# Kernel optimization log

Hardware: AMD Instinct MI355X
Metric: run time of the kernel (lower is better)

## Reference

```python
import jax, jax.numpy as jnp
import numpy as np

B, C, D, H, W = 4, 256, 16, 16, 16
REDUCTION = 8
CR = C // REDUCTION  # q/k channel dim = 32


def setup_inputs() -> dict:
    key = jax.random.key(0)
    k1, k2, k3, k4, k5, k6 = jax.random.split(key, 6)
    x = jax.random.normal(k1, (B, C, D, H, W), dtype=jnp.float32)
    # 1x1x1 conv weights are just [out_ch, in_ch] matrices
    Wq = jax.random.normal(k2, (CR, C), dtype=jnp.float32) * (1.0 / np.sqrt(C))
    Wk = jax.random.normal(k3, (CR, C), dtype=jnp.float32) * (1.0 / np.sqrt(C))
    Wv = jax.random.normal(k4, (C, C), dtype=jnp.float32) * (1.0 / np.sqrt(C))
    Wo = jax.random.normal(k5, (C, C), dtype=jnp.float32) * (1.0 / np.sqrt(C))
    gamma = jnp.zeros((1,), dtype=jnp.float32) + 0.5  # nonzero so output depends on attention
    return {"x": x, "Wq": Wq, "Wk": Wk, "Wv": Wv, "Wo": Wo, "gamma": gamma}


def reference(x, Wq, Wk, Wv, Wo, gamma):
    b, c, d, h, w = x.shape
    n = d * h * w
    scale = Wq.shape[0] ** -0.5  # (channels // reduction) ** -0.5
    xf = x.reshape(b, c, n)                      # [B, C, N]
    q = jnp.einsum('oc,bcn->bon', Wq, xf)        # [B, CR, N]
    k = jnp.einsum('oc,bcn->bon', Wk, xf)        # [B, CR, N]
    v = jnp.einsum('oc,bcn->bon', Wv, xf)        # [B, C, N]
    attn = jax.nn.softmax(jnp.einsum('bcn,bcm->bnm', q, k) * scale, axis=-1)  # [B, N, N]
    out = jnp.einsum('bcm,bnm->bcn', v, attn)    # v @ attn^T -> [B, C, N]
    out = jnp.einsum('oc,bcn->bon', Wo, out)     # output 1x1x1 conv
    out = out.reshape(b, c, d, h, w)
    return gamma[0] * out + x
```

## Files before the change

kernel.cpp:

```cpp
#include <hip/hip_runtime.h>
#include <hip/hip_bf16.h>

#define BATCH 4
#define CH 256
#define CRD 32
#define NN 4096

typedef __bf16 bf16x8 __attribute__((ext_vector_type(8)));
typedef float floatx4 __attribute__((ext_vector_type(4)));
typedef float floatx16 __attribute__((ext_vector_type(16)));
typedef unsigned short ushort4v __attribute__((ext_vector_type(4)));
typedef unsigned short ushort8v __attribute__((ext_vector_type(8)));
typedef unsigned int uint2v __attribute__((ext_vector_type(2)));
typedef unsigned int uint4v __attribute__((ext_vector_type(4)));

static __device__ __forceinline__ unsigned short f2bf(float f) {
    __bf16 h = (__bf16)f;
    return __builtin_bit_cast(unsigned short, h);
}
static __device__ __forceinline__ float bf2f(unsigned short h) {
    return __uint_as_float((unsigned int)h << 16);
}


__global__ __launch_bounds__(256) void wconv_kernel(
    const float* __restrict__ Wq, const float* __restrict__ Wk,
    const float* __restrict__ Wv, const float* __restrict__ Wo,
    unsigned short* __restrict__ What, unsigned short* __restrict__ WobF)
{
    const int o = blockIdx.x;
    const int t = threadIdx.x;
    float scale = 1.0f;
    const float* src;
    if (o < 32)      { src = Wq + o * 256;
                       scale = 0.17677669529663687f * 1.4426950408889634f; }
    else if (o < 64) { src = Wk + (o - 32) * 256; }
    else             { src = Wv + (o - 64) * 256; }
    const int mb = o >> 5;
    const size_t idx = ((size_t)(mb * 16 + (t >> 4)) * 64
                        + (o & 31) + 32 * ((t >> 3) & 1)) * 8 + (t & 7);
    What[idx] = f2bf(src[t] * scale);
    if (o < 256) {
        const size_t i2 = ((size_t)((o >> 5) * 16 + (t >> 4)) * 64
                           + (o & 31) + 32 * ((t >> 3) & 1)) * 8 + (t & 7);
        WobF[i2] = f2bf(Wo[o * 256 + t]);
    }
}

static __device__ __forceinline__ uint4v hmerge(
    const ushort4v& xp, const ushort4v& yp, int h)
{
    uint2v xd = __builtin_bit_cast(uint2v, xp);
    uint2v yd = __builtin_bit_cast(uint2v, yp);
    unsigned int px0 = (unsigned int)__shfl_xor((int)xd[0], 32);
    unsigned int px1 = (unsigned int)__shfl_xor((int)xd[1], 32);
    unsigned int py0 = (unsigned int)__shfl_xor((int)yd[0], 32);
    unsigned int py1 = (unsigned int)__shfl_xor((int)yd[1], 32);
    uint4v st;
    st[0] = h ? py0 : xd[0];
    st[1] = h ? py1 : xd[1];
    st[2] = h ? yd[0] : px0;
    st[3] = h ? yd[1] : px1;
    return st;
}

__global__ __launch_bounds__(640, 4) void qkv_kernel(
    const float* __restrict__ x, const unsigned short* __restrict__ What,
    unsigned short* __restrict__ qh, unsigned short* __restrict__ kh,
    unsigned short* __restrict__ vh)
{
    __shared__ __align__(16) unsigned short xf[16 * 512];

    const int t = threadIdx.x;
    const int w = t >> 6;
    const int l = t & 63;
    const int l31 = l & 31;
    const int h = l >> 5;
    const int nt = blockIdx.x, b = blockIdx.y;
    const int n0 = nt * 32;

    if (t < 512) {
        const float* xb = x + (size_t)(b * CH) * NN + n0;
        const int n = t & 31;
        const int cq = t >> 5;
        #pragma unroll
        for (int p = 0; p < 4; ++p) {
            int c = p * 64 + cq * 4;
            float v0 = xb[(size_t)(c + 0) * NN + n];
            float v1 = xb[(size_t)(c + 1) * NN + n];
            float v2 = xb[(size_t)(c + 2) * NN + n];
            float v3 = xb[(size_t)(c + 3) * NN + n];
            ushort4v u4;
            u4[0] = f2bf(v0); u4[1] = f2bf(v1); u4[2] = f2bf(v2); u4[3] = f2bf(v3);
            int addr = ((4 * p + (cq >> 2)) * 64 + n + 32 * ((cq >> 1) & 1)) * 8
                       + 4 * (cq & 1);
            *(ushort4v*)&xf[addr] = u4;
        }
    }
    __syncthreads();

    floatx16 acc;
    #pragma unroll
    for (int i = 0; i < 16; ++i) acc[i] = 0.f;

    for (int kblk = 0; kblk < 16; ++kblk) {
        bf16x8 bf = *(const bf16x8*)&xf[kblk * 512 + l * 8];
        bf16x8 af = *(const bf16x8*)(What + ((size_t)(w * 16 + kblk) * 64 + l) * 8);
        acc = __builtin_amdgcn_mfma_f32_32x32x16_bf16(af, bf, acc, 0, 0, 0);
    }

    auto store_qk = [&](unsigned short* dst, const floatx16& a) {
        size_t base = (size_t)(b * 128 + nt) * 1024;
        #pragma unroll
        for (int sb = 0; sb < 2; ++sb) {
            ushort4v xp, yp;
            #pragma unroll
            for (int i = 0; i < 4; ++i) {
                xp[i] = f2bf(a[8 * sb + i]);
                yp[i] = f2bf(a[8 * sb + 4 + i]);
            }
            uint4v st = hmerge(xp, yp, h);
            *(uint4v*)(dst + base + (size_t)sb * 512 + (size_t)l * 8) = st;
        }
    };

    if (w == 0)      store_qk(qh, acc);
    else if (w == 1) store_qk(kh, acc);

    __syncthreads();

    if (w >= 2) {
        const int cblk = w - 2;
        const int chunk = cblk * 2 + (l31 >> 4);
        const int hib = (l31 >> 3) & 1;
        #pragma unroll
        for (int r = 0; r < 16; ++r) {
            int rowo = (r & 3) + 8 * (r >> 2) + 4 * h;
            int unit = chunk * 64 + hib * 32 + rowo;
            int pu = unit ^ ((unit >> 5) & 7);
            xf[pu * 8 + (l31 & 7)] = f2bf(acc[r]);
        }
    }

    __syncthreads();

    if (t < 512) {
        #pragma unroll
        for (int p = 0; p < 2; ++p) {
            int Lu = p * 512 + t;
            int pu = Lu ^ ((Lu >> 5) & 7);
            uint4v d = *(const uint4v*)&xf[pu * 8];
            int chunk = Lu >> 6;
            int cblk = chunk >> 1, sub = chunk & 1;
            size_t dst = (((size_t)b * 8 + cblk) * 256 + nt * 2 + sub) * 512
                         + (size_t)(Lu & 63) * 8;
            *(uint4v*)(vh + dst) = d;
        }
    }
}

#define SM_M0 12.0f

__global__ __launch_bounds__(512, 4) void attn_kernel(
    const unsigned short* __restrict__ qh, const unsigned short* __restrict__ kh,
    const unsigned short* __restrict__ vh, unsigned short* __restrict__ Opart,
    float* __restrict__ ml)
{
    __shared__ unsigned short p_lds[2 * 16 * 64 * 8];
    __shared__ float psum_s[8][32];

    const int t = threadIdx.x;
    const int w = t >> 6;
    const int l = t & 63;
    const int l31 = l & 31;
    const int h = l >> 5;
    const int wk = w & 3;
    const int hq = w >> 2;

    const int lin = blockIdx.x + ((int)blockIdx.y << 6) + ((int)blockIdx.z << 7);
    const int combo = lin & 7;
    const int gp = lin >> 3;
    const int ks = combo & 1;
    const int b  = combo >> 1;
    const int g0 = 2 * gp, g1 = 2 * gp + 1;

    const unsigned short* qB = qh + (size_t)(b * 128 + (hq ? g1 : g0)) * 1024;
    const unsigned short* kB = kh + (size_t)b * 128 * 1024;
    const unsigned short* vB = vh + (size_t)b * 8 * 256 * 512;

    bf16x8 qf0 = *(const bf16x8*)(qB + l * 8);
    bf16x8 qf1 = *(const bf16x8*)(qB + 512 + l * 8);

    bf16x8 kf0 = *(const bf16x8*)(kB + (size_t)(ks * 64 + wk) * 1024 + l * 8);
    bf16x8 kf1 = *(const bf16x8*)(kB + (size_t)(ks * 64 + wk) * 1024 + 512 + l * 8);

    float l_loc = 0.f;
    floatx16 acc_a, acc_b;
    #pragma unroll
    for (int i = 0; i < 16; ++i) { acc_a[i] = 0.f; acc_b[i] = 0.f; }

    for (int it = 0; it < 16; ++it) {
        const int pbase = (it & 1) << 13;

        floatx16 sacc;
        #pragma unroll
        for (int i = 0; i < 16; ++i) sacc[i] = 0.f;
        __builtin_amdgcn_s_setprio(1);
        sacc = __builtin_amdgcn_mfma_f32_32x32x16_bf16(kf0, qf0, sacc, 0, 0, 0);
        sacc = __builtin_amdgcn_mfma_f32_32x32x16_bf16(kf1, qf1, sacc, 0, 0, 0);
        __builtin_amdgcn_s_setprio(0);

        float pv[16];
        #pragma unroll
        for (int r = 0; r < 16; ++r) pv[r] = __builtin_exp2f(sacc[r] - SM_M0);
        float s0 = (pv[0] + pv[1]) + (pv[2] + pv[3]);
        float s1 = (pv[4] + pv[5]) + (pv[6] + pv[7]);
        float s2 = (pv[8] + pv[9]) + (pv[10] + pv[11]);
        float s3 = (pv[12] + pv[13]) + (pv[14] + pv[15]);
        l_loc += (s0 + s1) + (s2 + s3);
        #pragma unroll
        for (int rg = 0; rg < 4; ++rg) {
            ushort4v pk;
            #pragma unroll
            for (int i = 0; i < 4; ++i) pk[i] = f2bf(pv[rg * 4 + i]);
            int idx = pbase
                    + ((hq * 8 + 2 * wk + (rg >> 1)) * 64
                       + l31 + 32 * (rg & 1)) * 8 + 4 * h;
            *(ushort4v*)&p_lds[idx] = pk;
        }
        if (it < 15) {
            const unsigned short* kn = kB + (size_t)(ks * 64 + (it + 1) * 4 + wk) * 1024;
            kf0 = *(const bf16x8*)(kn + l * 8);
            kf1 = *(const bf16x8*)(kn + 512 + l * 8);
        }
        const unsigned short* v0b = vB + ((size_t)w * 256 + (ks * 16 + it) * 8) * 512;
        bf16x8 va0 = *(const bf16x8*)(v0b + 0 * 512 + l * 8);
        bf16x8 va1 = *(const bf16x8*)(v0b + 1 * 512 + l * 8);
        bf16x8 va2 = *(const bf16x8*)(v0b + 2 * 512 + l * 8);
        bf16x8 va3 = *(const bf16x8*)(v0b + 3 * 512 + l * 8);
        bf16x8 va4 = *(const bf16x8*)(v0b + 4 * 512 + l * 8);
        bf16x8 va5 = *(const bf16x8*)(v0b + 5 * 512 + l * 8);
        bf16x8 va6 = *(const bf16x8*)(v0b + 6 * 512 + l * 8);
        bf16x8 va7 = *(const bf16x8*)(v0b + 7 * 512 + l * 8);

        __syncthreads();

        bf16x8 pa = *(const bf16x8*)&p_lds[pbase + l * 8];
        bf16x8 pb = *(const bf16x8*)&p_lds[pbase + 4096 + l * 8];
        #pragma unroll
        for (int s = 0; s < 8; ++s) {
            bf16x8 vcur = (s == 0) ? va0 : (s == 1) ? va1 : (s == 2) ? va2
                        : (s == 3) ? va3 : (s == 4) ? va4 : (s == 5) ? va5
                        : (s == 6) ? va6 : va7;
            bf16x8 pa_n, pb_n;
            if (s < 7) {
                pa_n = *(const bf16x8*)&p_lds[pbase + ((s + 1) * 64 + l) * 8];
                pb_n = *(const bf16x8*)&p_lds[pbase + 4096 + ((s + 1) * 64 + l) * 8];
            }
            __builtin_amdgcn_s_setprio(1);
            acc_a = __builtin_amdgcn_mfma_f32_32x32x16_bf16(vcur, pa, acc_a, 0, 0, 0);
            acc_b = __builtin_amdgcn_mfma_f32_32x32x16_bf16(vcur, pb, acc_b, 0, 0, 0);
            __builtin_amdgcn_s_setprio(0);
            pa = pa_n; pb = pb_n;
        }
    }

    float lt = l_loc + __shfl_xor(l_loc, 32);
    if (h == 0) psum_s[w][l31] = lt;
    __syncthreads();

    if (w == 0 && h == 0) {
        float l_run = (psum_s[0][l31] + psum_s[1][l31])
                    + (psum_s[2][l31] + psum_s[3][l31]);
        ml[((size_t)(b * 128 + g0) * 2 + ks) * 32 + l31] = l_run;
    }
    if (w == 4 && h == 0) {
        float l_run = (psum_s[4][l31] + psum_s[5][l31])
                    + (psum_s[6][l31] + psum_s[7][l31]);
        ml[((size_t)(b * 128 + g1) * 2 + ks) * 32 + l31] = l_run;
    }

    unsigned short* opa = Opart + ((size_t)((b * 128 + g0) * 2 + ks)) * 8192;
    unsigned short* opb = Opart + ((size_t)((b * 128 + g1) * 2 + ks)) * 8192;
    #pragma unroll
    for (int ct = 0; ct < 2; ++ct) {
        const floatx16& a = ct ? acc_b : acc_a;
        unsigned short* op = ct ? opb : opa;
        #pragma unroll
        for (int sb = 0; sb < 2; ++sb) {
            ushort4v xp, yp;
            #pragma unroll
            for (int i = 0; i < 4; ++i) {
                xp[i] = f2bf(a[8 * sb + i]);
                yp[i] = f2bf(a[8 * sb + 4 + i]);
            }
            uint4v st = hmerge(xp, yp, h);
            int sP = 2 * w + sb;
            *(uint4v*)(op + ((size_t)sP * 64 + l) * 8) = st;
        }
    }
}

__global__ __launch_bounds__(256, 4) void out_kernel(
    const unsigned short* __restrict__ Opart, const float* __restrict__ ml,
    const unsigned short* __restrict__ WobF, const float* __restrict__ x,
    const float* __restrict__ gamma, float* __restrict__ out)
{
    const int t = threadIdx.x;
    const int w = t >> 6;
    const int l = t & 63;
    const int l31 = l & 31;
    const int h = l >> 5;
    const int qt = blockIdx.x, mhalf = blockIdx.y, b = blockIdx.z;
    const int mt = mhalf * 4 + w;

    const size_t slot2 = (size_t)(b * 128 + qt) * 2;
    float l0 = ml[(slot2 + 0) * 32 + l31];
    float l1 = ml[(slot2 + 1) * 32 + l31];
    float rL = 1.0f / (l0 + l1);

    const unsigned short* o0 = Opart + (slot2 + 0) * 8192;
    const unsigned short* o1 = Opart + (slot2 + 1) * 8192;

    floatx16 a0, a1;
    #pragma unroll
    for (int i = 0; i < 16; ++i) { a0[i] = 0.f; a1[i] = 0.f; }

    for (int s = 0; s < 16; ++s) {
        bf16x8 f0 = *(const bf16x8*)(o0 + (s * 64 + l) * 8);
        bf16x8 f1 = *(const bf16x8*)(o1 + (s * 64 + l) * 8);
        bf16x8 af = *(const bf16x8*)(WobF + ((size_t)(mt * 16 + s) * 64 + l) * 8);
        a0 = __builtin_amdgcn_mfma_f32_32x32x16_bf16(af, f0, a0, 0, 0, 0);
        a1 = __builtin_amdgcn_mfma_f32_32x32x16_bf16(af, f1, a1, 0, 0, 0);
    }

    const float gm = gamma[0];
    #pragma unroll
    for (int r = 0; r < 16; ++r) {
        float v = (a0[r] + a1[r]) * rL;
        int o = mt * 32 + (r & 3) + 8 * (r >> 2) + 4 * h;
        int n = qt * 32 + l31;
        size_t oi = ((size_t)(b * 256 + o)) * NN + n;
        out[oi] = gm * v + x[oi];
    }
}

extern "C" void kernel_launch(void* const* d_in, const int* in_sizes, int n_in,
                              void* d_out, int out_size, void* d_ws, size_t ws_size,
                              hipStream_t stream)
{
    const float* x     = (const float*)d_in[0];
    const float* Wq    = (const float*)d_in[1];
    const float* Wk    = (const float*)d_in[2];
    const float* Wv    = (const float*)d_in[3];
    const float* Wo    = (const float*)d_in[4];
    const float* gamma = (const float*)d_in[5];
    float* out = (float*)d_out;

    char* wsb = (char*)d_ws;
    unsigned short* qh    = (unsigned short*)(wsb);
    unsigned short* kh    = (unsigned short*)(wsb + (1u << 20));
    unsigned short* vh    = (unsigned short*)(wsb + (2u << 20));
    unsigned short* What  = (unsigned short*)(wsb + (10u << 20));
    unsigned short* WobF  = (unsigned short*)(wsb + (10u << 20) + (256u << 10));
    unsigned short* Opart = (unsigned short*)(wsb + (11u << 20));
    float*          ml    = (float*)         (wsb + (45u << 20));

    wconv_kernel<<<320, 256, 0, stream>>>(Wq, Wk, Wv, Wo, What, WobF);

    dim3 g1(128, BATCH);
    qkv_kernel<<<g1, 640, 0, stream>>>(x, What, qh, kh, vh);

    dim3 g2(64, 2, BATCH);
    attn_kernel<<<g2, 512, 0, stream>>>(qh, kh, vh, Opart, ml);

    dim3 g3(128, 2, BATCH);
    out_kernel<<<g3, 256, 0, stream>>>(Opart, ml, WobF, x, gamma, out);
}
```

Baseline: 136.9 us.

## Fuse output projection into attention kernel and drop the key-split partials

Removes the two-way key split, so each attention block now loops over all 4096 keys. It normalizes the attention output in registers, stages it in LDS, and applies the Wo projection plus gamma residual directly, eliminating the separate out_kernel and the Opart/ml round trip through global memory. The cost is half as many attention blocks (256 instead of 512) with twice the serial work each. This may reduce parallelism and latency hiding on a large GPU, and the launch-bounds occupancy hint also changes.

```diff
diff --git a/kernel.cpp b/kernel.cpp
--- a/kernel.cpp
+++ b/kernel.cpp
@@ -161,10 +161,11 @@
 
 #define SM_M0 12.0f
 
-__global__ __launch_bounds__(512, 4) void attn_kernel(
+__global__ __launch_bounds__(512, 2) void attn_kernel(
     const unsigned short* __restrict__ qh, const unsigned short* __restrict__ kh,
-    const unsigned short* __restrict__ vh, unsigned short* __restrict__ Opart,
-    float* __restrict__ ml)
+    const unsigned short* __restrict__ vh, const unsigned short* __restrict__ WobF,
+    const float* __restrict__ x, const float* __restrict__ gamma,
+    float* __restrict__ out)
 {
     __shared__ unsigned short p_lds[2 * 16 * 64 * 8];
     __shared__ float psum_s[8][32];
@@ -177,11 +178,9 @@
     const int wk = w & 3;
     const int hq = w >> 2;
 
-    const int lin = blockIdx.x + ((int)blockIdx.y << 6) + ((int)blockIdx.z << 7);
-    const int combo = lin & 7;
-    const int gp = lin >> 3;
-    const int ks = combo & 1;
-    const int b  = combo >> 1;
+    const int lin = blockIdx.x + ((int)blockIdx.y << 6);
+    const int b  = (lin >> 1) & 3;
+    const int gp = ((lin >> 3) << 1) | (lin & 1);
     const int g0 = 2 * gp, g1 = 2 * gp + 1;
 
     const unsigned short* qB = qh + (size_t)(b * 128 + (hq ? g1 : g0)) * 1024;
@@ -191,15 +190,15 @@
     bf16x8 qf0 = *(const bf16x8*)(qB + l * 8);
     bf16x8 qf1 = *(const bf16x8*)(qB + 512 + l * 8);
 
-    bf16x8 kf0 = *(const bf16x8*)(kB + (size_t)(ks * 64 + wk) * 1024 + l * 8);
-    bf16x8 kf1 = *(const bf16x8*)(kB + (size_t)(ks * 64 + wk) * 1024 + 512 + l * 8);
+    bf16x8 kf0 = *(const bf16x8*)(kB + (size_t)wk * 1024 + l * 8);
+    bf16x8 kf1 = *(const bf16x8*)(kB + (size_t)wk * 1024 + 512 + l * 8);
 
     float l_loc = 0.f;
     floatx16 acc_a, acc_b;
     #pragma unroll
     for (int i = 0; i < 16; ++i) { acc_a[i] = 0.f; acc_b[i] = 0.f; }
 
-    for (int it = 0; it < 16; ++it) {
+    for (int it = 0; it < 32; ++it) {
         const int pbase = (it & 1) << 13;
 
         floatx16 sacc;
@@ -228,12 +227,12 @@
                        + l31 + 32 * (rg & 1)) * 8 + 4 * h;
             *(ushort4v*)&p_lds[idx] = pk;
         }
-        if (it < 15) {
-            const unsigned short* kn = kB + (size_t)(ks * 64 + (it + 1) * 4 + wk) * 1024;
+        if (it < 31) {
+            const unsigned short* kn = kB + (size_t)((it + 1) * 4 + wk) * 1024;
             kf0 = *(const bf16x8*)(kn + l * 8);
             kf1 = *(const bf16x8*)(kn + 512 + l * 8);
         }
-        const unsigned short* v0b = vB + ((size_t)w * 256 + (ks * 16 + it) * 8) * 512;
+        const unsigned short* v0b = vB + ((size_t)w * 256 + it * 8) * 512;
         bf16x8 va0 = *(const bf16x8*)(v0b + 0 * 512 + l * 8);
         bf16x8 va1 = *(const bf16x8*)(v0b + 1 * 512 + l * 8);
         bf16x8 va2 = *(const bf16x8*)(v0b + 2 * 512 + l * 8);
@@ -269,79 +268,54 @@
     if (h == 0) psum_s[w][l31] = lt;
     __syncthreads();
 
-    if (w == 0 && h == 0) {
-        float l_run = (psum_s[0][l31] + psum_s[1][l31])
-                    + (psum_s[2][l31] + psum_s[3][l31]);
-        ml[((size_t)(b * 128 + g0) * 2 + ks) * 32 + l31] = l_run;
-    }
-    if (w == 4 && h == 0) {
-        float l_run = (psum_s[4][l31] + psum_s[5][l31])
-                    + (psum_s[6][l31] + psum_s[7][l31]);
-        ml[((size_t)(b * 128 + g1) * 2 + ks) * 32 + l31] = l_run;
-    }
-
-    unsigned short* opa = Opart + ((size_t)((b * 128 + g0) * 2 + ks)) * 8192;
-    unsigned short* opb = Opart + ((size_t)((b * 128 + g1) * 2 + ks)) * 8192;
+    float rLa = 1.0f / ((psum_s[0][l31] + psum_s[1][l31])
+                      + (psum_s[2][l31] + psum_s[3][l31]));
+    float rLb = 1.0f / ((psum_s[4][l31] + psum_s[5][l31])
+                      + (psum_s[6][l31] + psum_s[7][l31]));
+
     #pragma unroll
     for (int ct = 0; ct < 2; ++ct) {
         const floatx16& a = ct ? acc_b : acc_a;
-        unsigned short* op = ct ? opb : opa;
+        const float rL = ct ? rLb : rLa;
+        const int obase = ct ? 8192 : 0;
         #pragma unroll
         for (int sb = 0; sb < 2; ++sb) {
             ushort4v xp, yp;
             #pragma unroll
             for (int i = 0; i < 4; ++i) {
-                xp[i] = f2bf(a[8 * sb + i]);
-                yp[i] = f2bf(a[8 * sb + 4 + i]);
+                xp[i] = f2bf(a[8 * sb + i] * rL);
+                yp[i] = f2bf(a[8 * sb + 4 + i] * rL);
             }
             uint4v st = hmerge(xp, yp, h);
-            int sP = 2 * w + sb;
-            *(uint4v*)(op + ((size_t)sP * 64 + l) * 8) = st;
-        }
-    }
-}
-
-__global__ __launch_bounds__(256, 4) void out_kernel(
-    const unsigned short* __restrict__ Opart, const float* __restrict__ ml,
-    const unsigned short* __restrict__ WobF, const float* __restrict__ x,
-    const float* __restrict__ gamma, float* __restrict__ out)
-{
-    const int t = threadIdx.x;
-    const int w = t >> 6;
-    const int l = t & 63;
-    const int l31 = l & 31;
-    const int h = l >> 5;
-    const int qt = blockIdx.x, mhalf = blockIdx.y, b = blockIdx.z;
-    const int mt = mhalf * 4 + w;
-
-    const size_t slot2 = (size_t)(b * 128 + qt) * 2;
-    float l0 = ml[(slot2 + 0) * 32 + l31];
-    float l1 = ml[(slot2 + 1) * 32 + l31];
-    float rL = 1.0f / (l0 + l1);
-
-    const unsigned short* o0 = Opart + (slot2 + 0) * 8192;
-    const unsigned short* o1 = Opart + (slot2 + 1) * 8192;
-
-    floatx16 a0, a1;
-    #pragma unroll
-    for (int i = 0; i < 16; ++i) { a0[i] = 0.f; a1[i] = 0.f; }
-
-    for (int s = 0; s < 16; ++s) {
-        bf16x8 f0 = *(const bf16x8*)(o0 + (s * 64 + l) * 8);
-        bf16x8 f1 = *(const bf16x8*)(o1 + (s * 64 + l) * 8);
-        bf16x8 af = *(const bf16x8*)(WobF + ((size_t)(mt * 16 + s) * 64 + l) * 8);
-        a0 = __builtin_amdgcn_mfma_f32_32x32x16_bf16(af, f0, a0, 0, 0, 0);
-        a1 = __builtin_amdgcn_mfma_f32_32x32x16_bf16(af, f1, a1, 0, 0, 0);
+            int kblk = 2 * w + sb;
+            *(uint4v*)&p_lds[obase + ((size_t)kblk * 64 + l) * 8] = st;
+        }
+    }
+    __syncthreads();
+
+    floatx16 oa, ob;
+    #pragma unroll
+    for (int i = 0; i < 16; ++i) { oa[i] = 0.f; ob[i] = 0.f; }
+    for (int kblk = 0; kblk < 16; ++kblk) {
+        bf16x8 af = *(const bf16x8*)(WobF + ((size_t)(w * 16 + kblk) * 64 + l) * 8);
+        bf16x8 ba = *(const bf16x8*)&p_lds[((size_t)kblk * 64 + l) * 8];
+        bf16x8 bb = *(const bf16x8*)&p_lds[8192 + ((size_t)kblk * 64 + l) * 8];
+        oa = __builtin_amdgcn_mfma_f32_32x32x16_bf16(af, ba, oa, 0, 0, 0);
+        ob = __builtin_amdgcn_mfma_f32_32x32x16_bf16(af, bb, ob, 0, 0, 0);
     }
 
     const float gm = gamma[0];
     #pragma unroll
-    for (int r = 0; r < 16; ++r) {
-        float v = (a0[r] + a1[r]) * rL;
-        int o = mt * 32 + (r & 3) + 8 * (r >> 2) + 4 * h;
-        int n = qt * 32 + l31;
-        size_t oi = ((size_t)(b * 256 + o)) * NN + n;
-        out[oi] = gm * v + x[oi];
+    for (int ct = 0; ct < 2; ++ct) {
+        const floatx16& a = ct ? ob : oa;
+        const int g = ct ? g1 : g0;
+        #pragma unroll
+        for (int r = 0; r < 16; ++r) {
+            int o = w * 32 + (r & 3) + 8 * (r >> 2) + 4 * h;
+            int n = g * 32 + l31;
+            size_t oi = ((size_t)(b * 256 + o)) * NN + n;
+            out[oi] = gm * a[r] + x[oi];
+        }
     }
 }
 
@@ -363,17 +337,12 @@
     unsigned short* vh    = (unsigned short*)(wsb + (2u << 20));
     unsigned short* What  = (unsigned short*)(wsb + (10u << 20));
     unsigned short* WobF  = (unsigned short*)(wsb + (10u << 20) + (256u << 10));
-    unsigned short* Opart = (unsigned short*)(wsb + (11u << 20));
-    float*          ml    = (float*)         (wsb + (45u << 20));
 
     wconv_kernel<<<320, 256, 0, stream>>>(Wq, Wk, Wv, Wo, What, WobF);
 
     dim3 g1(128, BATCH);
     qkv_kernel<<<g1, 640, 0, stream>>>(x, What, qh, kh, vh);
 
-    dim3 g2(64, 2, BATCH);
-    attn_kernel<<<g2, 512, 0, stream>>>(qh, kh, vh, Opart, ml);
-
-    dim3 g3(128, 2, BATCH);
-    out_kernel<<<g3, 256, 0, stream>>>(Opart, ml, WobF, x, gamma, out);
-}
+    dim3 g2(64, BATCH);
+    attn_kernel<<<g2, 512, 0, stream>>>(qh, kh, vh, WobF, x, gamma, out);
+}
```

Result: no change. 138.9 us (+1.4%).

## Software-pipeline QK^T/softmax one tile ahead of PV accumulation

Applied to the files above, without the earlier changes.

Restructures the attention loop so the QK^T MFMAs, exp2 softmax and P stores to LDS for tile it+1 are issued in the same iteration as the PV MFMAs for tile it. A prologue computes tile 0 before the loop, and the barrier moves to the end of each iteration, so the double-buffered P tile is still protected. The aim is to hide exp/convert latency and the barrier wait behind matrix work and give the scheduler more independent instructions. The cost is higher register pressure from keeping sacc and the V fragments live at the same time, plus one extra barrier.

```diff
diff --git a/kernel.cpp b/kernel.cpp
--- a/kernel.cpp
+++ b/kernel.cpp
@@ -191,25 +191,13 @@
     bf16x8 qf0 = *(const bf16x8*)(qB + l * 8);
     bf16x8 qf1 = *(const bf16x8*)(qB + 512 + l * 8);
 
-    bf16x8 kf0 = *(const bf16x8*)(kB + (size_t)(ks * 64 + wk) * 1024 + l * 8);
-    bf16x8 kf1 = *(const bf16x8*)(kB + (size_t)(ks * 64 + wk) * 1024 + 512 + l * 8);
-
     float l_loc = 0.f;
     floatx16 acc_a, acc_b;
     #pragma unroll
     for (int i = 0; i < 16; ++i) { acc_a[i] = 0.f; acc_b[i] = 0.f; }
 
-    for (int it = 0; it < 16; ++it) {
-        const int pbase = (it & 1) << 13;
-
-        floatx16 sacc;
-        #pragma unroll
-        for (int i = 0; i < 16; ++i) sacc[i] = 0.f;
-        __builtin_amdgcn_s_setprio(1);
-        sacc = __builtin_amdgcn_mfma_f32_32x32x16_bf16(kf0, qf0, sacc, 0, 0, 0);
-        sacc = __builtin_amdgcn_mfma_f32_32x32x16_bf16(kf1, qf1, sacc, 0, 0, 0);
-        __builtin_amdgcn_s_setprio(0);
-
+    auto softmax_store = [&](const floatx16& sacc, int j) {
+        const int pb = (j & 1) << 13;
         float pv[16];
         #pragma unroll
         for (int r = 0; r < 16; ++r) pv[r] = __builtin_exp2f(sacc[r] - SM_M0);
@@ -223,16 +211,43 @@
             ushort4v pk;
             #pragma unroll
             for (int i = 0; i < 4; ++i) pk[i] = f2bf(pv[rg * 4 + i]);
-            int idx = pbase
+            int idx = pb
                     + ((hq * 8 + 2 * wk + (rg >> 1)) * 64
                        + l31 + 32 * (rg & 1)) * 8 + 4 * h;
             *(ushort4v*)&p_lds[idx] = pk;
         }
+    };
+
+    bf16x8 kf0 = *(const bf16x8*)(kB + (size_t)(ks * 64 + wk) * 1024 + l * 8);
+    bf16x8 kf1 = *(const bf16x8*)(kB + (size_t)(ks * 64 + wk) * 1024 + 512 + l * 8);
+    {
+        floatx16 sacc;
+        #pragma unroll
+        for (int i = 0; i < 16; ++i) sacc[i] = 0.f;
+        sacc = __builtin_amdgcn_mfma_f32_32x32x16_bf16(kf0, qf0, sacc, 0, 0, 0);
+        sacc = __builtin_amdgcn_mfma_f32_32x32x16_bf16(kf1, qf1, sacc, 0, 0, 0);
+        softmax_store(sacc, 0);
+    }
+    {
+        const unsigned short* kn = kB + (size_t)(ks * 64 + 4 + wk) * 1024;
+        kf0 = *(const bf16x8*)(kn + l * 8);
+        kf1 = *(const bf16x8*)(kn + 512 + l * 8);
+    }
+    __syncthreads();
+
+    for (int it = 0; it < 16; ++it) {
+        const int pcur = (it & 1) << 13;
+
+        floatx16 sacc;
         if (it < 15) {
-            const unsigned short* kn = kB + (size_t)(ks * 64 + (it + 1) * 4 + wk) * 1024;
-            kf0 = *(const bf16x8*)(kn + l * 8);
-            kf1 = *(const bf16x8*)(kn + 512 + l * 8);
-        }
+            #pragma unroll
+            for (int i = 0; i < 16; ++i) sacc[i] = 0.f;
+            __builtin_amdgcn_s_setprio(1);
+            sacc = __builtin_amdgcn_mfma_f32_32x32x16_bf16(kf0, qf0, sacc, 0, 0, 0);
+            sacc = __builtin_amdgcn_mfma_f32_32x32x16_bf16(kf1, qf1, sacc, 0, 0, 0);
+            __builtin_amdgcn_s_setprio(0);
+        }
+
         const unsigned short* v0b = vB + ((size_t)w * 256 + (ks * 16 + it) * 8) * 512;
         bf16x8 va0 = *(const bf16x8*)(v0b + 0 * 512 + l * 8);
         bf16x8 va1 = *(const bf16x8*)(v0b + 1 * 512 + l * 8);
@@ -243,10 +258,17 @@
         bf16x8 va6 = *(const bf16x8*)(v0b + 6 * 512 + l * 8);
         bf16x8 va7 = *(const bf16x8*)(v0b + 7 * 512 + l * 8);
 
-        __syncthreads();
-
-        bf16x8 pa = *(const bf16x8*)&p_lds[pbase + l * 8];
-        bf16x8 pb = *(const bf16x8*)&p_lds[pbase + 4096 + l * 8];
+        if (it < 15) {
+            softmax_store(sacc, it + 1);
+            if (it < 14) {
+                const unsigned short* kn = kB + (size_t)(ks * 64 + (it + 2) * 4 + wk) * 1024;
+                kf0 = *(const bf16x8*)(kn + l * 8);
+                kf1 = *(const bf16x8*)(kn + 512 + l * 8);
+            }
+        }
+
+        bf16x8 pa = *(const bf16x8*)&p_lds[pcur + l * 8];
+        bf16x8 pb = *(const bf16x8*)&p_lds[pcur + 4096 + l * 8];
         #pragma unroll
         for (int s = 0; s < 8; ++s) {
             bf16x8 vcur = (s == 0) ? va0 : (s == 1) ? va1 : (s == 2) ? va2
@@ -254,8 +276,8 @@
                         : (s == 6) ? va6 : va7;
             bf16x8 pa_n, pb_n;
             if (s < 7) {
-                pa_n = *(const bf16x8*)&p_lds[pbase + ((s + 1) * 64 + l) * 8];
-                pb_n = *(const bf16x8*)&p_lds[pbase + 4096 + ((s + 1) * 64 + l) * 8];
+                pa_n = *(const bf16x8*)&p_lds[pcur + ((s + 1) * 64 + l) * 8];
+                pb_n = *(const bf16x8*)&p_lds[pcur + 4096 + ((s + 1) * 64 + l) * 8];
             }
             __builtin_amdgcn_s_setprio(1);
             acc_a = __builtin_amdgcn_mfma_f32_32x32x16_bf16(vcur, pa, acc_a, 0, 0, 0);
@@ -263,6 +285,8 @@
             __builtin_amdgcn_s_setprio(0);
             pa = pa_n; pb = pb_n;
         }
+
+        __syncthreads();
     }
 
     float lt = l_loc + __shfl_xor(l_loc, 32);
```

After: 136.2 us. No clear change (-0.5%).

## Retile attention to four query tiles per block with four-way key split

Applied to the files above, without the earlier changes.

Each attention block now covers four 32-query tiles and a quarter of the keys, instead of two query tiles and half the keys. Each loaded V fragment therefore feeds four MFMA accumulators rather than two, which halves the total V bytes read from global memory. The cost is twice as many partial outputs and row sums, which the output kernel now reads and reduces across four splits. The software prefetch of the next K tile is also dropped, so K loads now sit on the critical path of each iteration.

```diff
diff --git a/kernel.cpp b/kernel.cpp
--- a/kernel.cpp
+++ b/kernel.cpp
@@ -174,34 +174,35 @@
     const int l = t & 63;
     const int l31 = l & 31;
     const int h = l >> 5;
-    const int wk = w & 3;
-    const int hq = w >> 2;
-
-    const int lin = blockIdx.x + ((int)blockIdx.y << 6) + ((int)blockIdx.z << 7);
-    const int combo = lin & 7;
-    const int gp = lin >> 3;
-    const int ks = combo & 1;
-    const int b  = combo >> 1;
-    const int g0 = 2 * gp, g1 = 2 * gp + 1;
-
-    const unsigned short* qB = qh + (size_t)(b * 128 + (hq ? g1 : g0)) * 1024;
+    const int qq = w >> 1;
+    const int kslc = w & 1;
+
+    const int lin = blockIdx.x + ((int)blockIdx.y << 5) + ((int)blockIdx.z << 7);
+    const int slot = lin >> 3;
+    const int combo = ((lin & 7) << 1) | (slot >> 5);
+    const int qt = slot & 31;
+    const int ks = combo & 3;
+    const int b  = combo >> 2;
+
+    const unsigned short* qB = qh + (size_t)(b * 128 + qt * 4 + qq) * 1024;
     const unsigned short* kB = kh + (size_t)b * 128 * 1024;
     const unsigned short* vB = vh + (size_t)b * 8 * 256 * 512;
 
     bf16x8 qf0 = *(const bf16x8*)(qB + l * 8);
     bf16x8 qf1 = *(const bf16x8*)(qB + 512 + l * 8);
 
-    bf16x8 kf0 = *(const bf16x8*)(kB + (size_t)(ks * 64 + wk) * 1024 + l * 8);
-    bf16x8 kf1 = *(const bf16x8*)(kB + (size_t)(ks * 64 + wk) * 1024 + 512 + l * 8);
-
     float l_loc = 0.f;
-    floatx16 acc_a, acc_b;
-    #pragma unroll
-    for (int i = 0; i < 16; ++i) { acc_a[i] = 0.f; acc_b[i] = 0.f; }
+    floatx16 acc0, acc1, acc2, acc3;
+    #pragma unroll
+    for (int i = 0; i < 16; ++i) { acc0[i] = 0.f; acc1[i] = 0.f;
+                                   acc2[i] = 0.f; acc3[i] = 0.f; }
 
     for (int it = 0; it < 16; ++it) {
         const int pbase = (it & 1) << 13;
 
+        const unsigned short* kT = kB + (size_t)(ks * 32 + 2 * it + kslc) * 1024;
+        bf16x8 kf0 = *(const bf16x8*)(kT + l * 8);
+        bf16x8 kf1 = *(const bf16x8*)(kT + 512 + l * 8);
         floatx16 sacc;
         #pragma unroll
         for (int i = 0; i < 16; ++i) sacc[i] = 0.f;
@@ -224,44 +225,32 @@
             #pragma unroll
             for (int i = 0; i < 4; ++i) pk[i] = f2bf(pv[rg * 4 + i]);
             int idx = pbase
-                    + ((hq * 8 + 2 * wk + (rg >> 1)) * 64
+                    + ((qq * 4 + 2 * kslc + (rg >> 1)) * 64
                        + l31 + 32 * (rg & 1)) * 8 + 4 * h;
             *(ushort4v*)&p_lds[idx] = pk;
         }
-        if (it < 15) {
-            const unsigned short* kn = kB + (size_t)(ks * 64 + (it + 1) * 4 + wk) * 1024;
-            kf0 = *(const bf16x8*)(kn + l * 8);
-            kf1 = *(const bf16x8*)(kn + 512 + l * 8);
-        }
-        const unsigned short* v0b = vB + ((size_t)w * 256 + (ks * 16 + it) * 8) * 512;
-        bf16x8 va0 = *(const bf16x8*)(v0b + 0 * 512 + l * 8);
-        bf16x8 va1 = *(const bf16x8*)(v0b + 1 * 512 + l * 8);
-        bf16x8 va2 = *(const bf16x8*)(v0b + 2 * 512 + l * 8);
-        bf16x8 va3 = *(const bf16x8*)(v0b + 3 * 512 + l * 8);
-        bf16x8 va4 = *(const bf16x8*)(v0b + 4 * 512 + l * 8);
-        bf16x8 va5 = *(const bf16x8*)(v0b + 5 * 512 + l * 8);
-        bf16x8 va6 = *(const bf16x8*)(v0b + 6 * 512 + l * 8);
-        bf16x8 va7 = *(const bf16x8*)(v0b + 7 * 512 + l * 8);
+
+        const unsigned short* v0b = vB + ((size_t)w * 256 + (ks * 64 + it * 4)) * 512;
+        bf16x8 vs0 = *(const bf16x8*)(v0b + 0 * 512 + l * 8);
+        bf16x8 vs1 = *(const bf16x8*)(v0b + 1 * 512 + l * 8);
+        bf16x8 vs2 = *(const bf16x8*)(v0b + 2 * 512 + l * 8);
+        bf16x8 vs3 = *(const bf16x8*)(v0b + 3 * 512 + l * 8);
 
         __syncthreads();
 
-        bf16x8 pa = *(const bf16x8*)&p_lds[pbase + l * 8];
-        bf16x8 pb = *(const bf16x8*)&p_lds[pbase + 4096 + l * 8];
-        #pragma unroll
-        for (int s = 0; s < 8; ++s) {
-            bf16x8 vcur = (s == 0) ? va0 : (s == 1) ? va1 : (s == 2) ? va2
-                        : (s == 3) ? va3 : (s == 4) ? va4 : (s == 5) ? va5
-                        : (s == 6) ? va6 : va7;
-            bf16x8 pa_n, pb_n;
-            if (s < 7) {
-                pa_n = *(const bf16x8*)&p_lds[pbase + ((s + 1) * 64 + l) * 8];
-                pb_n = *(const bf16x8*)&p_lds[pbase + 4096 + ((s + 1) * 64 + l) * 8];
-            }
+        #pragma unroll
+        for (int s = 0; s < 4; ++s) {
+            bf16x8 vcur = (s == 0) ? vs0 : (s == 1) ? vs1 : (s == 2) ? vs2 : vs3;
+            bf16x8 p0 = *(const bf16x8*)&p_lds[pbase + ((0 * 4 + s) * 64 + l) * 8];
+            bf16x8 p1 = *(const bf16x8*)&p_lds[pbase + ((1 * 4 + s) * 64 + l) * 8];
+            bf16x8 p2 = *(const bf16x8*)&p_lds[pbase + ((2 * 4 + s) * 64 + l) * 8];
+            bf16x8 p3 = *(const bf16x8*)&p_lds[pbase + ((3 * 4 + s) * 64 + l) * 8];
             __builtin_amdgcn_s_setprio(1);
-            acc_a = __builtin_amdgcn_mfma_f32_32x32x16_bf16(vcur, pa, acc_a, 0, 0, 0);
-            acc_b = __builtin_amdgcn_mfma_f32_32x32x16_bf16(vcur, pb, acc_b, 0, 0, 0);
+            acc0 = __builtin_amdgcn_mfma_f32_32x32x16_bf16(vcur, p0, acc0, 0, 0, 0);
+            acc1 = __builtin_amdgcn_mfma_f32_32x32x16_bf16(vcur, p1, acc1, 0, 0, 0);
+            acc2 = __builtin_amdgcn_mfma_f32_32x32x16_bf16(vcur, p2, acc2, 0, 0, 0);
+            acc3 = __builtin_amdgcn_mfma_f32_32x32x16_bf16(vcur, p3, acc3, 0, 0, 0);
             __builtin_amdgcn_s_setprio(0);
-            pa = pa_n; pb = pb_n;
         }
     }
 
@@ -269,23 +258,18 @@
     if (h == 0) psum_s[w][l31] = lt;
     __syncthreads();
 
-    if (w == 0 && h == 0) {
-        float l_run = (psum_s[0][l31] + psum_s[1][l31])
-                    + (psum_s[2][l31] + psum_s[3][l31]);
-        ml[((size_t)(b * 128 + g0) * 2 + ks) * 32 + l31] = l_run;
-    }
-    if (w == 4 && h == 0) {
-        float l_run = (psum_s[4][l31] + psum_s[5][l31])
-                    + (psum_s[6][l31] + psum_s[7][l31]);
-        ml[((size_t)(b * 128 + g1) * 2 + ks) * 32 + l31] = l_run;
-    }
-
-    unsigned short* opa = Opart + ((size_t)((b * 128 + g0) * 2 + ks)) * 8192;
-    unsigned short* opb = Opart + ((size_t)((b * 128 + g1) * 2 + ks)) * 8192;
-    #pragma unroll
-    for (int ct = 0; ct < 2; ++ct) {
-        const floatx16& a = ct ? acc_b : acc_a;
-        unsigned short* op = ct ? opb : opa;
+    if ((w & 1) == 0 && h == 0) {
+        float l_run = psum_s[w][l31] + psum_s[w + 1][l31];
+        int myqq = w >> 1;
+        ml[((size_t)(b * 128 + qt * 4 + myqq) * 4 + ks) * 32 + l31] = l_run;
+    }
+
+    #pragma unroll
+    for (int cq = 0; cq < 4; ++cq) {
+        const floatx16& a = (cq == 0) ? acc0 : (cq == 1) ? acc1
+                          : (cq == 2) ? acc2 : acc3;
+        unsigned short* op = Opart
+            + ((size_t)((b * 128 + qt * 4 + cq) * 4 + ks)) * 8192;
         #pragma unroll
         for (int sb = 0; sb < 2; ++sb) {
             ushort4v xp, yp;
@@ -314,30 +298,36 @@
     const int qt = blockIdx.x, mhalf = blockIdx.y, b = blockIdx.z;
     const int mt = mhalf * 4 + w;
 
-    const size_t slot2 = (size_t)(b * 128 + qt) * 2;
-    float l0 = ml[(slot2 + 0) * 32 + l31];
-    float l1 = ml[(slot2 + 1) * 32 + l31];
-    float rL = 1.0f / (l0 + l1);
-
-    const unsigned short* o0 = Opart + (slot2 + 0) * 8192;
-    const unsigned short* o1 = Opart + (slot2 + 1) * 8192;
-
-    floatx16 a0, a1;
-    #pragma unroll
-    for (int i = 0; i < 16; ++i) { a0[i] = 0.f; a1[i] = 0.f; }
+    const size_t slot4 = (size_t)(b * 128 + qt) * 4;
+    float lsum = (ml[(slot4 + 0) * 32 + l31] + ml[(slot4 + 1) * 32 + l31])
+               + (ml[(slot4 + 2) * 32 + l31] + ml[(slot4 + 3) * 32 + l31]);
+    float rL = 1.0f / lsum;
+
+    const unsigned short* o0 = Opart + (slot4 + 0) * 8192;
+    const unsigned short* o1 = Opart + (slot4 + 1) * 8192;
+    const unsigned short* o2 = Opart + (slot4 + 2) * 8192;
+    const unsigned short* o3 = Opart + (slot4 + 3) * 8192;
+
+    floatx16 acc;
+    #pragma unroll
+    for (int i = 0; i < 16; ++i) acc[i] = 0.f;
 
     for (int s = 0; s < 16; ++s) {
+        bf16x8 af = *(const bf16x8*)(WobF + ((size_t)(mt * 16 + s) * 64 + l) * 8);
         bf16x8 f0 = *(const bf16x8*)(o0 + (s * 64 + l) * 8);
         bf16x8 f1 = *(const bf16x8*)(o1 + (s * 64 + l) * 8);
-        bf16x8 af = *(const bf16x8*)(WobF + ((size_t)(mt * 16 + s) * 64 + l) * 8);
-        a0 = __builtin_amdgcn_mfma_f32_32x32x16_bf16(af, f0, a0, 0, 0, 0);
-        a1 = __builtin_amdgcn_mfma_f32_32x32x16_bf16(af, f1, a1, 0, 0, 0);
+        bf16x8 f2 = *(const bf16x8*)(o2 + (s * 64 + l) * 8);
+        bf16x8 f3 = *(const bf16x8*)(o3 + (s * 64 + l) * 8);
+        acc = __builtin_amdgcn_mfma_f32_32x32x16_bf16(af, f0, acc, 0, 0, 0);
+        acc = __builtin_amdgcn_mfma_f32_32x32x16_bf16(af, f1, acc, 0, 0, 0);
+        acc = __builtin_amdgcn_mfma_f32_32x32x16_bf16(af, f2, acc, 0, 0, 0);
+        acc = __builtin_amdgcn_mfma_f32_32x32x16_bf16(af, f3, acc, 0, 0, 0);
     }
 
     const float gm = gamma[0];
     #pragma unroll
     for (int r = 0; r < 16; ++r) {
-        float v = (a0[r] + a1[r]) * rL;
+        float v = acc[r] * rL;
         int o = mt * 32 + (r & 3) + 8 * (r >> 2) + 4 * h;
         int n = qt * 32 + l31;
         size_t oi = ((size_t)(b * 256 + o)) * NN + n;
@@ -371,7 +361,7 @@
     dim3 g1(128, BATCH);
     qkv_kernel<<<g1, 640, 0, stream>>>(x, What, qh, kh, vh);
 
-    dim3 g2(64, 2, BATCH);
+    dim3 g2(32, 4, BATCH);
     attn_kernel<<<g2, 512, 0, stream>>>(qh, kh, vh, Opart, ml);
 
     dim3 g3(128, 2, BATCH);
```

Result: slower. 140.8 us (+2.8%).
